# Kernel optimization log

Hardware: AMD Instinct MI355X
Metric: run time of the kernel (lower is better)

The kernel has to match this reference:

```python
import jax, jax.numpy as jnp
import numpy as np

D_MODEL = 1024
N_HEADS = 16
D_HIDDEN = 4096
EPS = 1e-6
MASK_VAL = 1e10


def layernorm(x, gamma, beta):
    # Matches torch module: unbiased std (N-1), divide by (std + eps)
    mean = jnp.mean(x, axis=-1, keepdims=True)
    d = x.shape[-1]
    std = jnp.sqrt(jnp.sum((x - mean) ** 2, axis=-1, keepdims=True) / (d - 1))
    return gamma * (x - mean) / (std + EPS) + beta


def multihead(q_in, k_in, v_in, wq, wk, wv, wo, causal):
    # nn.Linear(bias=False): y = x @ W.T
    q = q_in @ wq.T
    k = k_in @ wk.T
    v = v_in @ wv.T
    B, Sq, D = q.shape
    Sk = k.shape[1]
    H, dh = N_HEADS, D // N_HEADS
    q = q.reshape(B, Sq, H, dh)
    k = k.reshape(B, Sk, H, dh)
    v = v.reshape(B, Sk, H, dh)
    scores = jnp.einsum('bqhd,bkhd->bhqk', q, k)  # [B,H,Sq,Sk]
    if causal:
        tri = jnp.triu(jnp.full((Sk, Sk), MASK_VAL, dtype=scores.dtype), k=1)
        scores = scores - tri  # mask applied BEFORE scaling, as in source
    scale = jnp.sqrt(jnp.asarray(D_MODEL, dtype=scores.dtype))  # d_key = d_model
    att = jax.nn.softmax(scores / scale, axis=-1)
    out = jnp.einsum('bhqk,bkhd->bqhd', att, v).reshape(B, Sq, D)
    return out @ wo.T


def setup_inputs() -> dict:
    key = jax.random.key(0)
    ks = jax.random.split(key, 24)
    B, S, D, DH = 2, 2048, D_MODEL, D_HIDDEN
    w = lambda k, shp: (jax.random.normal(k, shp, dtype=jnp.float32) * 0.02)
    inp = {
        'x': jax.random.normal(ks[0], (B, S, D), dtype=jnp.float32),
        'encoding': jax.random.normal(ks[1], (B, S, D), dtype=jnp.float32),
        'sa_wq': w(ks[2], (D, D)), 'sa_wk': w(ks[3], (D, D)),
        'sa_wv': w(ks[4], (D, D)), 'sa_wo': w(ks[5], (D, D)),
        'ca_wq': w(ks[6], (D, D)), 'ca_wk': w(ks[7], (D, D)),
        'ca_wv': w(ks[8], (D, D)), 'ca_wo': w(ks[9], (D, D)),
        'ff_w1': w(ks[10], (DH, D)), 'ff_b1': jnp.zeros((DH,), jnp.float32),
        'ff_w2': w(ks[11], (D, DH)), 'ff_b2': jnp.zeros((D,), jnp.float32),
        'ln1_g': jnp.ones((D,), jnp.float32), 'ln1_b': jnp.zeros((D,), jnp.float32),
        'ln2_g': jnp.ones((D,), jnp.float32), 'ln2_b': jnp.zeros((D,), jnp.float32),
        'ln3_g': jnp.ones((D,), jnp.float32), 'ln3_b': jnp.zeros((D,), jnp.float32),
    }
    return inp


def reference(x, encoding, sa_wq, sa_wk, sa_wv, sa_wo, ca_wq, ca_wk, ca_wv, ca_wo,
              ff_w1, ff_b1, ff_w2, ff_b2, ln1_g, ln1_b, ln2_g, ln2_b, ln3_g, ln3_b):
    # self-attention (causal) + post-norm residual
    h = layernorm(x + multihead(x, x, x, sa_wq, sa_wk, sa_wv, sa_wo, causal=True), ln1_g, ln1_b)
    # cross-attention + post-norm residual
    h = layernorm(h + multihead(h, encoding, encoding, ca_wq, ca_wk, ca_wv, ca_wo, causal=False), ln2_g, ln2_b)
    # feed-forward + post-norm residual
    ff = jax.nn.relu(h @ ff_w1.T + ff_b1) @ ff_w2.T + ff_b2
    return layernorm(h + ff, ln3_g, ln3_b)
```

## Files before the change

kernel.cpp:

```cpp
#include <hip/hip_runtime.h>
#include <hip/hip_bf16.h>
#include <math.h>

#define D_MODEL 1024
#define NHEADS  16
#define DHEAD   64
#define D_HID   4096

typedef __attribute__((ext_vector_type(8))) short short8;
typedef __attribute__((ext_vector_type(4))) short short4v;
typedef __attribute__((ext_vector_type(4))) float f32x4;
typedef __attribute__((ext_vector_type(16))) float f32x16;

#define QSCALE_F 0.04508422002778011f
#define MASK_T   4.5084220e8f

__device__ inline short f2bs(float x) {
    union { __hip_bfloat16 b; short s; } u;
    u.b = __float2bfloat16(x);
    return u.s;
}
__device__ inline float bs2f(ushort s) {
    union { unsigned u; float f; } v; v.u = ((unsigned)s) << 16; return v.f;
}
__device__ inline unsigned cvtpk(float lo, float hi) {
    unsigned r;
    asm("v_cvt_pk_bf16_f32 %0, %1, %2" : "=v"(r) : "v"(lo), "v"(hi));
    return r;
}
__device__ inline short8 pack8(float4 x, float4 y) {
    short8 v;
    v[0] = f2bs(x.x); v[1] = f2bs(x.y); v[2] = f2bs(x.z); v[3] = f2bs(x.w);
    v[4] = f2bs(y.x); v[5] = f2bs(y.y); v[6] = f2bs(y.z); v[7] = f2bs(y.w);
    return v;
}
typedef const unsigned __attribute__((address_space(1))) gu32;
typedef unsigned __attribute__((address_space(3))) lu32;
__device__ inline void gload16(const void* g, void* l) {
    __builtin_amdgcn_global_load_lds((gu32*)g, (lu32*)l, 16, 0, 0);
}
__device__ inline int swz(int r, int byteInRow) {
    return (r * 128 + byteInRow) ^ ((r & 7) << 4);
}

struct WP { const float* p[10]; };
__global__ __launch_bounds__(256) void cast_weights(WP wp, short* __restrict__ dst) {
    const int n8 = (16 << 20) / 8;
    for (int i = blockIdx.x * 256 + threadIdx.x; i < n8; i += gridDim.x * 256) {
        size_t e = (size_t)i * 8;
        int seg = (int)(e >> 20);
        const float* src;
        if (seg < 8)       src = wp.p[seg] + (e & ((1u << 20) - 1));
        else if (seg < 12) src = wp.p[8] + (e - ((size_t)8 << 20));
        else               src = wp.p[9] + (e - ((size_t)12 << 20));
        float4 a = *(const float4*)src;
        float4 b = *(const float4*)(src + 4);
        *(short8*)(dst + e) = pack8(a, b);
    }
}

__global__ __launch_bounds__(256) void cast_f2b(const float* __restrict__ in,
                                                short* __restrict__ out, int n8) {
    for (int i = blockIdx.x * 256 + threadIdx.x; i < n8; i += gridDim.x * 256) {
        float4 a = *(const float4*)(in + (size_t)i * 8);
        float4 b = *(const float4*)(in + (size_t)i * 8 + 4);
        *(short8*)(out + (size_t)i * 8) = pack8(a, b);
    }
}

template<int OM, bool BIAS, bool RELU, bool ACCUM>
__global__ __launch_bounds__(256) void gemm_mfma(
    const short* __restrict__ A, int lda,
    const short* __restrict__ Bm, int ldb,
    const float* __restrict__ bias,
    float* __restrict__ Cf, short* __restrict__ Cb, int ldc,
    int M, int N, int K, size_t routeElems, float qscale)
{
    __shared__ short Als[128 * 64];
    __shared__ short Bls[128 * 64];

    const int tid = threadIdx.x, w = tid >> 6, l = tid & 63;
    const int l15 = l & 15, lhi = l >> 4;
    const int wr = w >> 1, wc = w & 1;

    const int kh = (OM == 3) ? blockIdx.z : 0;
    if (OM == 3) {
        A  += (size_t)kh * K;
        Bm += (size_t)kh * K;
    }

    const unsigned nwg  = gridDim.x * gridDim.y;
    const unsigned wgid = blockIdx.y * gridDim.x + blockIdx.x;
    const unsigned cpx  = nwg >> 3;
    const unsigned sid  = (wgid & 7) * cpx + (wgid >> 3);
    const int bm = (int)(sid / gridDim.x) * 128;
    const int bn = (int)(sid % gridDim.x) * 128;

    const int srow = w * 8 + (l >> 3);
    const int schk = ((l & 7) ^ (l >> 3)) * 8;

    f32x4 acc[4][4] = {};

    for (int k0 = 0; k0 < K; k0 += 64) {
        #pragma unroll
        for (int i = 0; i < 4; ++i) {
            const short* ga = A  + (size_t)(bm + i * 32 + srow) * lda + k0 + schk;
            const short* gb = Bm + (size_t)(bn + i * 32 + srow) * ldb + k0 + schk;
            gload16(ga, &Als[i * 2048 + w * 512]);
            gload16(gb, &Bls[i * 2048 + w * 512]);
        }
        __syncthreads();

        short8 af[4][2], bf[4][2];
        #pragma unroll
        for (int m = 0; m < 4; ++m) {
            const int row = wr * 64 + m * 16 + l15;
            #pragma unroll
            for (int kk = 0; kk < 2; ++kk)
                af[m][kk] = *(const short8*)&Als[row * 64 + (((kk * 4 + lhi) ^ (l15 & 7)) * 8)];
        }
        #pragma unroll
        for (int n = 0; n < 4; ++n) {
            const int row = wc * 64 + n * 16 + l15;
            #pragma unroll
            for (int kk = 0; kk < 2; ++kk)
                bf[n][kk] = *(const short8*)&Bls[row * 64 + (((kk * 4 + lhi) ^ (l15 & 7)) * 8)];
        }
        #pragma unroll
        for (int kk = 0; kk < 2; ++kk)
            #pragma unroll
            for (int m = 0; m < 4; ++m)
                #pragma unroll
                for (int n = 0; n < 4; ++n)
                    acc[m][n] = __builtin_amdgcn_mfma_f32_16x16x32_bf16(af[m][kk], bf[n][kk], acc[m][n], 0, 0, 0);
        __syncthreads();
    }

    #pragma unroll
    for (int n = 0; n < 4; ++n) {
        const int col = bn + wc * 64 + n * 16 + l15;
        float bv = 0.f;
        if (BIAS && (OM != 3 || kh == 0)) bv = bias[col];
        const float sc = (OM == 2) ? (col < 1024 ? qscale : 1.f) : qscale;
        #pragma unroll
        for (int m = 0; m < 4; ++m) {
            const int row0 = bm + wr * 64 + m * 16 + lhi * 4;
            #pragma unroll
            for (int i = 0; i < 4; ++i) {
                float v = acc[m][n][i] + bv;
                if (ACCUM) v += Cf[(size_t)(row0 + i) * ldc + col];
                if (RELU)  v = fmaxf(v, 0.f);
                v *= sc;
                if (OM == 0) {
                    Cf[(size_t)(row0 + i) * ldc + col] = v;
                } else if (OM == 1) {
                    Cb[(size_t)(row0 + i) * ldc + col] = f2bs(v);
                } else if (OM == 2) {
                    Cb[(size_t)(col >> 10) * routeElems +
                       (size_t)(row0 + i) * 1024 + (col & 1023)] = f2bs(v);
                } else {
                    if (kh == 0) Cf[(size_t)(row0 + i) * ldc + col] = v;
                    else         Cb[(size_t)(row0 + i) * ldc + col] = f2bs(v);
                }
            }
        }
    }
}

__global__ __launch_bounds__(256) void v_prep(
    const short* __restrict__ Vb_, short* __restrict__ Vt, int S)
{
    const int t = blockIdx.x, bh = blockIdx.y;
    const int b = bh >> 4, h = bh & 15;
    const int tid = threadIdx.x;
    const int r = tid >> 2, g = tid & 3;
    __shared__ ushort vs[64][65];

    const size_t inrow = ((size_t)b * S + t * 64 + r) * D_MODEL + h * DHEAD;
    const size_t tbase = ((size_t)bh * (S / 64) + t) * 4096;

    short8 v0 = *(const short8*)(Vb_ + inrow + g * 16);
    short8 v1 = *(const short8*)(Vb_ + inrow + g * 16 + 8);
    #pragma unroll
    for (int j = 0; j < 8; ++j) { vs[r][g * 16 + j] = (ushort)v0[j]; vs[r][g * 16 + 8 + j] = (ushort)v1[j]; }
    __syncthreads();
    short8 q0, q1;
    #pragma unroll
    for (int j = 0; j < 8; ++j) {
        q0[j] = (short)vs[g * 16 + j][r];
        q1[j] = (short)vs[g * 16 + 8 + j][r];
    }
    *(short8*)(Vt + tbase + r * 64 + g * 16)     = q0;
    *(short8*)(Vt + tbase + r * 64 + g * 16 + 8) = q1;
}

template<bool CAUSAL>
__global__ __launch_bounds__(256, 3) void attn_v10(
    const short* __restrict__ Qb, const short* __restrict__ Kr,
    const short* __restrict__ Vt, short* __restrict__ Out, int S)
{
    __shared__ __align__(16) char smem[2 * 16384];

    const int tid = threadIdx.x, w = tid >> 6, l = tid & 63;
    const int l31 = l & 31, hi = l >> 5;
    const int bnd = blockIdx.x;
    const int bh = blockIdx.y, b = bh >> 4, h = bh & 15;
    const int qw = bnd * 128 + w * 32;
    const int q  = qw + l31;

    const short* qp = Qb + ((size_t)(b * S + q)) * 1024 + h * 64 + hi * 8;
    short8 bq[4];
    #pragma unroll
    for (int dc = 0; dc < 4; ++dc) bq[dc] = *(const short8*)(qp + dc * 16);

    const short* kbase = Kr + ((size_t)b * S) * 1024 + h * 64;
    const short* vbase = Vt + (size_t)bh * ((S / 64) * 4096);

    f32x16 ot0 = {}, ot1 = {};
    float l_lane = 0.f;

    const int tMax = CAUSAL ? (2 * bnd + 1) : (S / 64 - 1);
    const int sr = tid >> 2, sc = tid & 3;

    short8 gk0, gk1, gv0, gv1;
    {
        const short* kg = kbase + (size_t)(sr) * 1024 + sc * 8;
        const short* vg = vbase + sr * 64 + sc * 8;
        gk0 = *(const short8*)kg;        gk1 = *(const short8*)(kg + 32);
        gv0 = *(const short8*)vg;        gv1 = *(const short8*)(vg + 32);
    }
    {
        char* Kls = smem;            char* Vls = smem + 8192;
        *(short8*)(Kls + swz(sr, sc * 16))      = gk0;
        *(short8*)(Kls + swz(sr, sc * 16 + 64)) = gk1;
        *(short8*)(Vls + swz(sr, sc * 16))      = gv0;
        *(short8*)(Vls + swz(sr, sc * 16 + 64)) = gv1;
    }
    __syncthreads();

    int cur = 0;
    for (int t = 0; t <= tMax; ++t) {
        const bool hasNext = (t + 1 <= tMax);
        if (hasNext) {
            const short* kg = kbase + (size_t)((t + 1) * 64 + sr) * 1024 + sc * 8;
            const short* vg = vbase + (size_t)(t + 1) * 4096 + sr * 64 + sc * 8;
            gk0 = *(const short8*)kg;    gk1 = *(const short8*)(kg + 32);
            gv0 = *(const short8*)vg;    gv1 = *(const short8*)(vg + 32);
        }

        const char* Kls = smem + cur * 16384;
        const char* Vls = Kls + 8192;
        const int kv0 = t * 64;

        if (!(CAUSAL && kv0 > qw + 31)) {
            f32x16 st0 = {}, st1 = {};
            __builtin_amdgcn_s_setprio(1);
            #pragma unroll
            for (int dc = 0; dc < 4; ++dc) {
                short8 a0 = *(const short8*)(Kls + swz(l31,      dc * 32 + hi * 16));
                short8 a1 = *(const short8*)(Kls + swz(32 + l31, dc * 32 + hi * 16));
                st0 = __builtin_amdgcn_mfma_f32_32x32x16_bf16(a0, bq[dc], st0, 0, 0, 0);
                st1 = __builtin_amdgcn_mfma_f32_32x32x16_bf16(a1, bq[dc], st1, 0, 0, 0);
            }
            __builtin_amdgcn_s_setprio(0);

            if (CAUSAL && kv0 + 31 > qw) {
                #pragma unroll
                for (int r = 0; r < 16; ++r) {
                    int kv = kv0 + (r & 3) + 8 * (r >> 2) + 4 * hi;
                    if (kv > q) st0[r] -= MASK_T;
                }
            }
            if (CAUSAL && kv0 + 63 > qw) {
                #pragma unroll
                for (int r = 0; r < 16; ++r) {
                    int kv = kv0 + 32 + (r & 3) + 8 * (r >> 2) + 4 * hi;
                    if (kv > q) st1[r] -= MASK_T;
                }
            }

            union U { unsigned u[4]; short8 s; };
            U c00, c01, c10, c11;
            {
                float p[16];
                #pragma unroll
                for (int r = 0; r < 16; ++r) { p[r] = __builtin_amdgcn_exp2f(st0[r]); l_lane += p[r]; }
                unsigned wd[8], sx[8];
                #pragma unroll
                for (int i = 0; i < 8; ++i) wd[i] = cvtpk(p[2 * i], p[2 * i + 1]);
                #pragma unroll
                for (int i = 0; i < 8; ++i) sx[i] = __shfl_xor(wd[i], 32, 64);
                if (hi == 0) {
                    c00.u[0] = wd[0]; c00.u[1] = wd[1]; c00.u[2] = sx[0]; c00.u[3] = sx[1];
                    c01.u[0] = wd[4]; c01.u[1] = wd[5]; c01.u[2] = sx[4]; c01.u[3] = sx[5];
                } else {
                    c00.u[0] = sx[2]; c00.u[1] = sx[3]; c00.u[2] = wd[2]; c00.u[3] = wd[3];
                    c01.u[0] = sx[6]; c01.u[1] = sx[7]; c01.u[2] = wd[6]; c01.u[3] = wd[7];
                }
            }
            {
                float p[16];
                #pragma unroll
                for (int r = 0; r < 16; ++r) { p[r] = __builtin_amdgcn_exp2f(st1[r]); l_lane += p[r]; }
                unsigned wd[8], sx[8];
                #pragma unroll
                for (int i = 0; i < 8; ++i) wd[i] = cvtpk(p[2 * i], p[2 * i + 1]);
                #pragma unroll
                for (int i = 0; i < 8; ++i) sx[i] = __shfl_xor(wd[i], 32, 64);
                if (hi == 0) {
                    c10.u[0] = wd[0]; c10.u[1] = wd[1]; c10.u[2] = sx[0]; c10.u[3] = sx[1];
                    c11.u[0] = wd[4]; c11.u[1] = wd[5]; c11.u[2] = sx[4]; c11.u[3] = sx[5];
                } else {
                    c10.u[0] = sx[2]; c10.u[1] = sx[3]; c10.u[2] = wd[2]; c10.u[3] = wd[3];
                    c11.u[0] = sx[6]; c11.u[1] = sx[7]; c11.u[2] = wd[6]; c11.u[3] = wd[7];
                }
            }

            __builtin_amdgcn_s_setprio(1);
            short8 av;
            av  = *(const short8*)(Vls + swz(l31,      hi * 16));
            ot0 = __builtin_amdgcn_mfma_f32_32x32x16_bf16(av, c00.s, ot0, 0, 0, 0);
            av  = *(const short8*)(Vls + swz(32 + l31, hi * 16));
            ot1 = __builtin_amdgcn_mfma_f32_32x32x16_bf16(av, c00.s, ot1, 0, 0, 0);
            av  = *(const short8*)(Vls + swz(l31,      32 + hi * 16));
            ot0 = __builtin_amdgcn_mfma_f32_32x32x16_bf16(av, c01.s, ot0, 0, 0, 0);
            av  = *(const short8*)(Vls + swz(32 + l31, 32 + hi * 16));
            ot1 = __builtin_amdgcn_mfma_f32_32x32x16_bf16(av, c01.s, ot1, 0, 0, 0);
            av  = *(const short8*)(Vls + swz(l31,      64 + hi * 16));
            ot0 = __builtin_amdgcn_mfma_f32_32x32x16_bf16(av, c10.s, ot0, 0, 0, 0);
            av  = *(const short8*)(Vls + swz(32 + l31, 64 + hi * 16));
            ot1 = __builtin_amdgcn_mfma_f32_32x32x16_bf16(av, c10.s, ot1, 0, 0, 0);
            av  = *(const short8*)(Vls + swz(l31,      96 + hi * 16));
            ot0 = __builtin_amdgcn_mfma_f32_32x32x16_bf16(av, c11.s, ot0, 0, 0, 0);
            av  = *(const short8*)(Vls + swz(32 + l31, 96 + hi * 16));
            ot1 = __builtin_amdgcn_mfma_f32_32x32x16_bf16(av, c11.s, ot1, 0, 0, 0);
            __builtin_amdgcn_s_setprio(0);
        }

        if (hasNext) {
            char* Kn = smem + (cur ^ 1) * 16384;
            char* Vn = Kn + 8192;
            *(short8*)(Kn + swz(sr, sc * 16))      = gk0;
            *(short8*)(Kn + swz(sr, sc * 16 + 64)) = gk1;
            *(short8*)(Vn + swz(sr, sc * 16))      = gv0;
            *(short8*)(Vn + swz(sr, sc * 16 + 64)) = gv1;
        }
        __syncthreads();
        cur ^= 1;
    }

    const float l_tot = l_lane + __shfl_xor(l_lane, 32, 64);
    const float inv = 1.f / l_tot;
    short* orow = Out + ((size_t)(b * S + q)) * 1024 + h * 64;
    #pragma unroll
    for (int i = 0; i < 8; ++i) {
        int dbase = ((2 * i) & 3) + 8 * (i >> 1) + 4 * hi;
        *(unsigned*)(orow + dbase)      = cvtpk(ot0[2 * i] * inv, ot0[2 * i + 1] * inv);
        *(unsigned*)(orow + 32 + dbase) = cvtpk(ot1[2 * i] * inv, ot1[2 * i + 1] * inv);
    }
}

template<bool IN1BF, bool OUTBF, bool P3>
__global__ __launch_bounds__(256) void add_ln(
    const void* __restrict__ in1, const float* __restrict__ in2,
    const short* __restrict__ in3,
    const float* __restrict__ gam, const float* __restrict__ bet,
    void* __restrict__ y)
{
    const int row = blockIdx.x;
    const int tid = threadIdx.x;
    const size_t off = (size_t)row * D_MODEL;

    float a0, a1, a2, a3;
    if (IN1BF) {
        short4v xs = ((const short4v*)((const short*)in1 + off))[tid];
        a0 = bs2f((ushort)xs[0]); a1 = bs2f((ushort)xs[1]);
        a2 = bs2f((ushort)xs[2]); a3 = bs2f((ushort)xs[3]);
    } else {
        float4 xv = ((const float4*)((const float*)in1 + off))[tid];
        a0 = xv.x; a1 = xv.y; a2 = xv.z; a3 = xv.w;
    }
    float4 rv = ((const float4*)(in2 + off))[tid];
    float v0 = a0 + rv.x, v1 = a1 + rv.y, v2 = a2 + rv.z, v3 = a3 + rv.w;
    if (P3) {
        short4v ps = ((const short4v*)(in3 + off))[tid];
        v0 += bs2f((ushort)ps[0]); v1 += bs2f((ushort)ps[1]);
        v2 += bs2f((ushort)ps[2]); v3 += bs2f((ushort)ps[3]);
    }

    float s  = v0 + v1 + v2 + v3;
    float ss = v0 * v0 + v1 * v1 + v2 * v2 + v3 * v3;

    __shared__ float sb[8];
    #pragma unroll
    for (int o = 32; o > 0; o >>= 1) {
        s  += __shfl_down(s, o, 64);
        ss += __shfl_down(ss, o, 64);
    }
    const int lane = tid & 63, w = tid >> 6;
    if (lane == 0) { sb[w] = s; sb[4 + w] = ss; }
    __syncthreads();
    float S  = sb[0] + sb[1] + sb[2] + sb[3];
    float SS = sb[4] + sb[5] + sb[6] + sb[7];

    float mean = S * (1.f / D_MODEL);
    float var_sum = SS - S * mean;
    float stdv = sqrtf(var_sum * (1.f / (D_MODEL - 1)));
    float inv = 1.f / (stdv + 1e-6f);

    float4 gv = ((const float4*)gam)[tid];
    float4 bv = ((const float4*)bet)[tid];
    float o0 = gv.x * (v0 - mean) * inv + bv.x;
    float o1 = gv.y * (v1 - mean) * inv + bv.y;
    float o2 = gv.z * (v2 - mean) * inv + bv.z;
    float o3 = gv.w * (v3 - mean) * inv + bv.w;
    if (OUTBF) {
        short4v ov; ov[0] = f2bs(o0); ov[1] = f2bs(o1); ov[2] = f2bs(o2); ov[3] = f2bs(o3);
        ((short4v*)((short*)y + off))[tid] = ov;
    } else {
        ((float4*)((float*)y + off))[tid] = make_float4(o0, o1, o2, o3);
    }
}

extern "C" void kernel_launch(void* const* d_in, const int* in_sizes, int n_in,
                              void* d_out, int out_size, void* d_ws, size_t ws_size,
                              hipStream_t stream)
{
    const float* x     = (const float*)d_in[0];
    const float* enc   = (const float*)d_in[1];
    WP wp;
    for (int i = 0; i < 8; ++i) wp.p[i] = (const float*)d_in[2 + i];
    wp.p[8] = (const float*)d_in[10];
    wp.p[9] = (const float*)d_in[12];
    const float* ff_b1 = (const float*)d_in[11];
    const float* ff_b2 = (const float*)d_in[13];
    const float* ln1_g = (const float*)d_in[14];
    const float* ln1_b = (const float*)d_in[15];
    const float* ln2_g = (const float*)d_in[16];
    const float* ln2_b = (const float*)d_in[17];
    const float* ln3_g = (const float*)d_in[18];
    const float* ln3_b = (const float*)d_in[19];
    float* out = (float*)d_out;

    const int Bn = 2, S = 2048, M = Bn * S;
    const size_t MB = 1u << 20;
    char* ws = (char*)d_ws;
    short* Wb   = (short*)(ws);
    short* p32  = (short*)(ws + 32 * MB);
    short* p40  = (short*)(ws + 40 * MB);
    short* p48  = (short*)(ws + 48 * MB);
    short* p56  = (short*)(ws + 56 * MB);
    short* p64  = (short*)(ws + 64 * MB);
    short* p72  = (short*)(ws + 72 * MB);
    float* f0   = (float*)(ws + 80 * MB);

    short* tbuf = p48;

    const size_t RT = 4 * MB;
    const short* W_saqkv = Wb;
    const short* W_sawo  = Wb + 3 * MB;
    const short* W_caq   = Wb + 4 * MB;
    const short* W_cakv  = Wb + 5 * MB;
    const short* W_cawo  = Wb + 7 * MB;
    const short* W_ff1   = Wb + 8 * MB;
    const short* W_ff2   = Wb + 12 * MB;

    dim3 blk(256);
    dim3 g_qkv(3072 / 128, M / 128);
    dim3 g_kv(2048 / 128, M / 128);
    dim3 g_n1k(1024 / 128, M / 128);
    dim3 g_spl(1024 / 128, M / 128, 2);
    dim3 g_ff1(4096 / 128, M / 128);
    dim3 g_attn(S / 128, Bn * NHEADS);
    dim3 g_vp(S / 64, Bn * NHEADS);
    dim3 g_ln(M);

    cast_weights<<<2048, blk, 0, stream>>>(wp, Wb);
    cast_f2b<<<2048, blk, 0, stream>>>(x, p32, (M * D_MODEL) / 8);

    gemm_mfma<2,false,false,false><<<g_qkv, blk, 0, stream>>>(p32, 1024, W_saqkv, 1024, nullptr, nullptr, p40, 1024, M, 3072, 1024, RT, QSCALE_F);
    v_prep<<<g_vp, blk, 0, stream>>>(p56, p72, S);
    attn_v10<true><<<g_attn, blk, 0, stream>>>(p40, p48, p72, p32, S);
    gemm_mfma<3,false,false,false><<<g_spl, blk, 0, stream>>>(p32, 1024, W_sawo, 1024, nullptr, f0, p48, 1024, M, 1024, 512, 0, 1.f);
    add_ln<false,true,true><<<g_ln, blk, 0, stream>>>(x, f0, p48, ln1_g, ln1_b, p32);

    cast_f2b<<<2048, blk, 0, stream>>>(enc, p64, (M * D_MODEL) / 8);
    gemm_mfma<2,false,false,false><<<g_kv, blk, 0, stream>>>(p64, 1024, W_cakv, 1024, nullptr, nullptr, p48, 1024, M, 2048, 1024, RT, 1.f);
    gemm_mfma<1,false,false,false><<<g_n1k, blk, 0, stream>>>(p32, 1024, W_caq, 1024, nullptr, nullptr, p40, 1024, M, 1024, 1024, 0, QSCALE_F);
    v_prep<<<g_vp, blk, 0, stream>>>(p56, p72, S);
    attn_v10<false><<<g_attn, blk, 0, stream>>>(p40, p48, p72, p56, S);
    gemm_mfma<3,false,false,false><<<g_spl, blk, 0, stream>>>(p56, 1024, W_cawo, 1024, nullptr, f0, p48, 1024, M, 1024, 512, 0, 1.f);
    add_ln<true,true,true><<<g_ln, blk, 0, stream>>>(p32, f0, p48, ln2_g, ln2_b, p40);

    gemm_mfma<1,true,true,false><<<g_ff1, blk, 0, stream>>>(p40, 1024, W_ff1, 1024, ff_b1, nullptr, tbuf, 4096, M, 4096, 1024, 0, 1.f);
    gemm_mfma<3,true,false,false><<<g_spl, blk, 0, stream>>>(tbuf, 4096, W_ff2, 4096, ff_b2, f0, p32, 1024, M, 1024, 2048, 0, 1.f);
    add_ln<true,false,true><<<g_ln, blk, 0, stream>>>(p40, f0, p32, ln3_g, ln3_b, out);
}
```

Before: 374.6 us.

## Double-buffer GEMM LDS tiles and raise wave priority around MFMA block

The MFMA GEMM now uses two LDS buffers for the A and B tiles. It issues the global-to-LDS loads for the next K slice before computing on the current one, so load latency overlaps with matrix math and one barrier per iteration is dropped. It also raises wave priority during the MFMA burst with s_setprio. The trade-off is doubled LDS use (64KB per block), which may lower occupancy.

```diff
diff --git a/kernel.cpp b/kernel.cpp
--- a/kernel.cpp
+++ b/kernel.cpp
@@ -76,8 +76,8 @@
     float* __restrict__ Cf, short* __restrict__ Cb, int ldc,
     int M, int N, int K, size_t routeElems, float qscale)
 {
-    __shared__ short Als[128 * 64];
-    __shared__ short Bls[128 * 64];
+    __shared__ short Als[2][128 * 64];
+    __shared__ short Bls[2][128 * 64];
 
     const int tid = threadIdx.x, w = tid >> 6, l = tid & 63;
     const int l15 = l & 15, lhi = l >> 4;
@@ -101,15 +101,28 @@
 
     f32x4 acc[4][4] = {};
 
-    for (int k0 = 0; k0 < K; k0 += 64) {
-        #pragma unroll
-        for (int i = 0; i < 4; ++i) {
-            const short* ga = A  + (size_t)(bm + i * 32 + srow) * lda + k0 + schk;
-            const short* gb = Bm + (size_t)(bn + i * 32 + srow) * ldb + k0 + schk;
-            gload16(ga, &Als[i * 2048 + w * 512]);
-            gload16(gb, &Bls[i * 2048 + w * 512]);
-        }
-        __syncthreads();
+    #pragma unroll
+    for (int i = 0; i < 4; ++i) {
+        const short* ga = A  + (size_t)(bm + i * 32 + srow) * lda + schk;
+        const short* gb = Bm + (size_t)(bn + i * 32 + srow) * ldb + schk;
+        gload16(ga, &Als[0][i * 2048 + w * 512]);
+        gload16(gb, &Bls[0][i * 2048 + w * 512]);
+    }
+    __syncthreads();
+
+    const int nIter = K >> 6;
+    int cur = 0;
+    for (int it = 0; it < nIter; ++it) {
+        if (it + 1 < nIter) {
+            const int k1 = (it + 1) << 6;
+            #pragma unroll
+            for (int i = 0; i < 4; ++i) {
+                const short* ga = A  + (size_t)(bm + i * 32 + srow) * lda + k1 + schk;
+                const short* gb = Bm + (size_t)(bn + i * 32 + srow) * ldb + k1 + schk;
+                gload16(ga, &Als[cur ^ 1][i * 2048 + w * 512]);
+                gload16(gb, &Bls[cur ^ 1][i * 2048 + w * 512]);
+            }
+        }
 
         short8 af[4][2], bf[4][2];
         #pragma unroll
@@ -117,15 +130,16 @@
             const int row = wr * 64 + m * 16 + l15;
             #pragma unroll
             for (int kk = 0; kk < 2; ++kk)
-                af[m][kk] = *(const short8*)&Als[row * 64 + (((kk * 4 + lhi) ^ (l15 & 7)) * 8)];
+                af[m][kk] = *(const short8*)&Als[cur][row * 64 + (((kk * 4 + lhi) ^ (l15 & 7)) * 8)];
         }
         #pragma unroll
         for (int n = 0; n < 4; ++n) {
             const int row = wc * 64 + n * 16 + l15;
             #pragma unroll
             for (int kk = 0; kk < 2; ++kk)
-                bf[n][kk] = *(const short8*)&Bls[row * 64 + (((kk * 4 + lhi) ^ (l15 & 7)) * 8)];
-        }
+                bf[n][kk] = *(const short8*)&Bls[cur][row * 64 + (((kk * 4 + lhi) ^ (l15 & 7)) * 8)];
+        }
+        __builtin_amdgcn_s_setprio(1);
         #pragma unroll
         for (int kk = 0; kk < 2; ++kk)
             #pragma unroll
@@ -133,7 +147,10 @@
                 #pragma unroll
                 for (int n = 0; n < 4; ++n)
                     acc[m][n] = __builtin_amdgcn_mfma_f32_16x16x32_bf16(af[m][kk], bf[n][kk], acc[m][n], 0, 0, 0);
+        __builtin_amdgcn_s_setprio(0);
+
         __syncthreads();
+        cur ^= 1;
     }
 
     #pragma unroll
```

New measurement: 360.5 us. 1.04x faster.
